# Optimization experiments

Measured on AMD Instinct MI355X. Metric: run time of the kernel, lower is better.

Reference implementation:

```python
import jax, jax.numpy as jnp
import numpy as np

TAU = 2.0      # LIF membrane time constant
VTH = 1.0      # spiking threshold (spikingjelly default)
ALPHA = 4.0    # surrogate sigmoid sharpness (spikingjelly Sigmoid default)
EPS = 1e-5     # BatchNorm eps


@jax.custom_vjp
def spike(v):
    # Heaviside(v) with surrogate sigmoid gradient
    return (v >= 0.0).astype(v.dtype)

def _spike_fwd(v):
    return spike(v), v

def _spike_bwd(v, g):
    s = jax.nn.sigmoid(ALPHA * v)
    return (g * ALPHA * s * (1.0 - s),)

spike.defvjp(_spike_fwd, _spike_bwd)


def lif(x_seq):
    # MultiStepLIFNode: x_seq [T, B, C], v_reset=0 (hard reset), detach_reset=True
    def step(v, xt):
        v = v + (xt - v) / TAU           # membrane decay + charge
        s = spike(v - VTH)               # fire
        v = v * (1.0 - jax.lax.stop_gradient(s))  # detached hard reset to 0
        return v, s
    v0 = jnp.zeros_like(x_seq[0])
    _, s_seq = jax.lax.scan(step, v0, x_seq)
    return s_seq


def block(h, w, b, gamma, beta):
    # h: [B, C_in, T] -> conv1d(k=3, pad=1) -> BN (batch stats) -> LIF -> [B, E, T]
    y = jax.lax.conv_general_dilated(h, w, window_strides=(1,), padding=[(1, 1)],
                                     dimension_numbers=('NCH', 'OIH', 'NCH'))
    y = y + b[None, :, None]
    mu = y.mean(axis=(0, 2), keepdims=True)
    var = y.var(axis=(0, 2), keepdims=True)
    y = (y - mu) * jax.lax.rsqrt(var + EPS) * gamma[None, :, None] + beta[None, :, None]
    s = lif(jnp.transpose(y, (2, 0, 1)))        # [T, B, E]
    return jnp.transpose(s, (1, 2, 0))          # [B, E, T]


def setup_inputs() -> dict:
    key = jax.random.key(0)
    ks = jax.random.split(key, 8)
    B, T, Cin, E, O = 64, 1024, 8, 256, 63
    return {
        'x':       jax.random.normal(ks[0], (B, T, Cin), jnp.float32),
        'conv0_w': jax.random.normal(ks[1], (E, Cin, 3), jnp.float32) * (1.0 / np.sqrt(Cin * 3)),
        'conv0_b': jax.random.normal(ks[2], (E,), jnp.float32) * 0.01,
        'convs_w': jax.random.normal(ks[3], (3, E, E, 3), jnp.float32) * (1.0 / np.sqrt(E * 3)),
        'convs_b': jax.random.normal(ks[4], (3, E), jnp.float32) * 0.01,
        'bn_gamma': jnp.ones((4, E), jnp.float32),
        'bn_beta':  jnp.zeros((4, E), jnp.float32),
        'head_w':  jax.random.normal(ks[5], (O, E), jnp.float32) * (1.0 / np.sqrt(E)),
        'head_b':  jnp.zeros((O,), jnp.float32),
    }


def reference(x, conv0_w, conv0_b, convs_w, convs_b, bn_gamma, bn_beta, head_w, head_b):
    h = jnp.transpose(x, (0, 2, 1))  # [B, C, T]
    h = block(h, conv0_w, conv0_b, bn_gamma[0], bn_beta[0])
    for i in range(convs_w.shape[0]):
        h = block(h, convs_w[i], convs_b[i], bn_gamma[i + 1], bn_beta[i + 1])
    h = h.mean(axis=-1)  # AdaptiveAvgPool1d(1) + squeeze -> [B, E]
    return h @ head_w.T + head_b  # [B, O]
```

## Files before the change

### kernel.cpp

```cpp
#include <hip/hip_runtime.h>
#include <hip/hip_bf16.h>
#include <stdint.h>

#define NB 64
#define NT 1024
#define CIN 8
#define NE 256
#define NO 63
#define TPAD 16
#define TROWS (NT + 2*TPAD)
#define LCH 128
#define LWU 48
#define TT 256

using bf16x8 = __attribute__((ext_vector_type(8))) short;
using f32x4  = __attribute__((ext_vector_type(4))) float;

__global__ void conv0_prep(const float* __restrict__ x, const float* __restrict__ w0,
                           const float* __restrict__ b0, float* __restrict__ y,
                           float* __restrict__ part,
                           const float* __restrict__ cw, __hip_bfloat16* __restrict__ wfr) {
    int bid = blockIdx.x;
    if (bid >= 512) {
        int F = (bid - 512) * 256 + threadIdx.x;
        int lane = F & 63;
        int xx = F >> 6;
        int cph = xx & 7;  xx >>= 3;
        int e4  = xx & 15; xx >>= 4;
        int s   = xx & 1;  xx >>= 1;
        int k   = xx % 3;
        int l   = xx / 3;
        int e = e4*16 + (lane & 15);
        int cb = cph*32 + (lane >> 4)*8;
        __hip_bfloat16 outv[8];
        #pragma unroll
        for (int j = 0; j < 8; ++j) {
            float w = cw[((size_t)(l*256 + e)*256 + (cb + j))*3 + k];
            __hip_bfloat16 hi = __float2bfloat16(w);
            if (s == 0) outv[j] = hi;
            else        outv[j] = __float2bfloat16(w - __bfloat162float(hi));
        }
        *(uint4*)(wfr + (size_t)F*8) = *(uint4*)outv;
        return;
    }
    int b = bid >> 3, tc = bid & 7;
    int e = threadIdx.x;
    int t0 = tc * 128;
    __shared__ float xs[1040];
    for (int i = threadIdx.x; i < 1040; i += 256) {
        int t = t0 - 1 + (i >> 3); int c = i & 7;
        xs[i] = (t >= 0 && t < NT) ? x[((size_t)b*NT + t)*CIN + c] : 0.0f;
    }
    __syncthreads();
    float w[24];
    #pragma unroll
    for (int j = 0; j < 24; ++j) w[j] = w0[e*24 + j];
    float bias = b0[e];
    float s = 0.0f, qq = 0.0f;
    for (int dt = 0; dt < 128; ++dt) {
        float acc = bias;
        #pragma unroll
        for (int c = 0; c < 8; ++c)
            #pragma unroll
            for (int k = 0; k < 3; ++k)
                acc += xs[(dt + k)*8 + c] * w[c*3 + k];
        y[((size_t)b*NT + t0 + dt)*NE + e] = acc;
        s += acc; qq += acc*acc;
    }
    int p = b*8 + tc;
    part[(size_t)p*512 + e]       = s;
    part[(size_t)p*512 + 256 + e] = qq;
}

__global__ void stats_final(const float* __restrict__ part, const float* __restrict__ gamma,
                            const float* __restrict__ beta, float4* __restrict__ lifp, int np) {
    int e = blockIdx.x; int lane = threadIdx.x;
    double s = 0.0, q = 0.0;
    for (int p = lane; p < np; p += 64) {
        s += (double)part[(size_t)p*512 + e];
        q += (double)part[(size_t)p*512 + 256 + e];
    }
    #pragma unroll
    for (int off = 1; off < 64; off <<= 1) {
        s += __shfl_xor(s, off, 64);
        q += __shfl_xor(q, off, 64);
    }
    if (lane == 0) {
        const double N = 65536.0;
        double mean = s / N;
        double var  = q / N - mean*mean;
        float rs = (float)(1.0 / sqrt(var + 1e-5));
        float4 o; o.x = (float)mean; o.y = rs * gamma[e]; o.z = beta[e]; o.w = 0.0f;
        lifp[e] = o;
    }
}

template<bool WS>
__global__ void lif_kern(const float* __restrict__ y, const float4* __restrict__ lifp,
                         __hip_bfloat16* __restrict__ S, float* __restrict__ pool) {
    int c = blockIdx.x, b = blockIdx.y;
    int e = threadIdx.x;
    float4 pr = lifp[e];
    float mu = pr.x, rsg = pr.y, bet = pr.z;
    const __hip_bfloat16 z   = __float2bfloat16(0.0f);
    const __hip_bfloat16 one = __float2bfloat16(1.0f);
    if (WS) {
        if (c == 0) {
            for (int r = 0; r < TPAD; ++r) S[((size_t)b*TROWS + r)*NE + e] = z;
        }
        if (c == 7) {
            for (int r = 0; r < TPAD; ++r) S[((size_t)b*TROWS + TPAD + NT + r)*NE + e] = z;
        }
    }
    int t0 = c * LCH;
    int tw = t0 - LWU; if (tw < 0) tw = 0;
    const float* yb = y + (size_t)b*NT*NE + e;
    __hip_bfloat16* sb = S + ((size_t)b*TROWS + TPAD)*NE + e;
    float v = 0.0f;
    #pragma unroll 8
    for (int t = tw; t < t0; ++t) {
        float xx = yb[(size_t)t*NE];
        float yn = (xx - mu)*rsg + bet;
        float d  = __fsub_rn(yn, v);
        v = __fadd_rn(v, __fmul_rn(d, 0.5f));
        v = (v >= 1.0f) ? 0.0f : v;
    }
    float cnt = 0.0f;
    #pragma unroll 8
    for (int t = t0; t < t0 + LCH; ++t) {
        float xx = yb[(size_t)t*NE];
        float yn = (xx - mu)*rsg + bet;
        float d  = __fsub_rn(yn, v);
        v = __fadd_rn(v, __fmul_rn(d, 0.5f));
        bool sp = (v >= 1.0f);
        if (WS) sb[(size_t)t*NE] = sp ? one : z;
        else    cnt += sp ? 1.0f : 0.0f;
        v = sp ? 0.0f : v;
    }
    if (!WS) pool[(size_t)(b*8 + c)*256 + e] = cnt;
}

__global__ __launch_bounds__(256, 2) void conv_mfma(
    const __hip_bfloat16* __restrict__ Sp,
    const __hip_bfloat16* __restrict__ Wfr,
    const float* __restrict__ bias,
    float* __restrict__ y,
    float* __restrict__ part)
{
    __shared__ short Bbuf[260*32];
    const int tid  = threadIdx.x;
    const int wave = tid >> 6, lane = tid & 63;
    const int n16  = lane & 15, q = lane >> 4;
    const int we = wave & 1, wt = wave >> 1;
    const int tt = blockIdx.x, et = blockIdx.y, b = blockIdx.z;
    const int t0 = tt * TT;

    f32x4 acc[4][8] = {};
    bf16x8 bfr[8];

    const __hip_bfloat16* Sbase = Sp + ((size_t)b*TROWS + (TPAD - 1 + t0)) * NE;

    for (int ph = 0; ph < 8; ++ph) {
        const int c0 = ph * 32;
        __syncthreads();
        for (int idx = tid; idx < 258*4; idx += 256) {
            int r = idx >> 2, sg = idx & 3;
            uint4 d = *(const uint4*)(Sbase + (size_t)r*NE + c0 + sg*8);
            int sgs = sg ^ ((r >> 1) & 3);
            *(uint4*)((char*)Bbuf + r*64 + sgs*16) = d;
        }
        __syncthreads();
        #pragma unroll 1
        for (int kk = 0; kk < 3; ++kk) {
            #pragma unroll
            for (int g = 0; g < 8; ++g) {
                int row = wt*128 + g*16 + n16 + kk;
                int sgs = q ^ ((row >> 1) & 3);
                bfr[g] = *(const bf16x8*)((const char*)Bbuf + row*64 + sgs*16);
            }
            #pragma unroll
            for (int s = 0; s < 2; ++s) {
                const __hip_bfloat16* wb = Wfr
                    + ((((size_t)(kk*2 + s)*16 + (et*8 + we*4))*8 + ph) << 9) + lane*8;
                bf16x8 afr[4];
                #pragma unroll
                for (int f = 0; f < 4; ++f)
                    afr[f] = *(const bf16x8*)(wb + ((size_t)f << 12));
                #pragma unroll
                for (int f = 0; f < 4; ++f)
                    #pragma unroll
                    for (int g = 0; g < 8; ++g)
                        acc[f][g] = __builtin_amdgcn_mfma_f32_16x16x32_bf16(afr[f], bfr[g], acc[f][g], 0, 0, 0);
            }
        }
    }

    float ls[16] = {}, lq[16] = {};
    float4 bv[4];
    #pragma unroll
    for (int f = 0; f < 4; ++f) bv[f] = *(const float4*)(bias + et*128 + we*64 + f*16 + q*4);
    #pragma unroll
    for (int g = 0; g < 8; ++g) {
        int t = t0 + wt*128 + g*16 + n16;
        float* yt = y + ((size_t)b*NT + t)*NE + et*128 + we*64 + q*4;
        #pragma unroll
        for (int f = 0; f < 4; ++f) {
            f32x4 a = acc[f][g];
            float4 o;
            o.x = a[0] + bv[f].x; o.y = a[1] + bv[f].y; o.z = a[2] + bv[f].z; o.w = a[3] + bv[f].w;
            *(float4*)(yt + f*16) = o;
            ls[f*4+0] += o.x; lq[f*4+0] += o.x*o.x;
            ls[f*4+1] += o.y; lq[f*4+1] += o.y*o.y;
            ls[f*4+2] += o.z; lq[f*4+2] += o.z*o.z;
            ls[f*4+3] += o.w; lq[f*4+3] += o.w*o.w;
        }
    }
    #pragma unroll
    for (int off = 1; off < 16; off <<= 1) {
        #pragma unroll
        for (int i = 0; i < 16; ++i) {
            ls[i] += __shfl_xor(ls[i], off, 64);
            lq[i] += __shfl_xor(lq[i], off, 64);
        }
    }
    __syncthreads();
    float* red = (float*)Bbuf;
    if (n16 == 0 && wt == 0) {
        #pragma unroll
        for (int f = 0; f < 4; ++f)
            #pragma unroll
            for (int r = 0; r < 4; ++r) {
                int el = we*64 + f*16 + q*4 + r;
                red[el] = ls[f*4+r]; red[128+el] = lq[f*4+r];
            }
    }
    __syncthreads();
    if (n16 == 0 && wt == 1) {
        #pragma unroll
        for (int f = 0; f < 4; ++f)
            #pragma unroll
            for (int r = 0; r < 4; ++r) {
                int el = we*64 + f*16 + q*4 + r;
                red[el] += ls[f*4+r]; red[128+el] += lq[f*4+r];
            }
    }
    __syncthreads();
    if (tid < 128) {
        int p = b*4 + tt;
        part[(size_t)p*512 + et*128 + tid]       = red[tid];
        part[(size_t)p*512 + 256 + et*128 + tid] = red[128 + tid];
    }
}

__global__ void head_final(const float* __restrict__ pool, const float* __restrict__ hw,
                           const float* __restrict__ hb, float* __restrict__ out) {
    int b = blockIdx.x;
    int tid = threadIdx.x;
    __shared__ float pooled[256];
    float s = 0.0f;
    #pragma unroll
    for (int c = 0; c < 8; ++c) s += pool[(size_t)(b*8 + c)*256 + tid];
    pooled[tid] = s * (1.0f/1024.0f);
    __syncthreads();
    if (tid < NO) {
        float acc = hb[tid];
        for (int c = 0; c < 256; ++c) acc += pooled[c] * hw[tid*256 + c];
        out[b*NO + tid] = acc;
    }
}

extern "C" void kernel_launch(void* const* d_in, const int* in_sizes, int n_in,
                              void* d_out, int out_size, void* d_ws, size_t ws_size,
                              hipStream_t stream) {
    (void)in_sizes; (void)n_in; (void)out_size; (void)ws_size;
    const float* x       = (const float*)d_in[0];
    const float* conv0_w = (const float*)d_in[1];
    const float* conv0_b = (const float*)d_in[2];
    const float* convs_w = (const float*)d_in[3];
    const float* convs_b = (const float*)d_in[4];
    const float* bn_g    = (const float*)d_in[5];
    const float* bn_b    = (const float*)d_in[6];
    const float* head_w  = (const float*)d_in[7];
    const float* head_b  = (const float*)d_in[8];
    float* out = (float*)d_out;

    char* ws = (char*)d_ws;
    float*          y      = (float*)ws;
    __hip_bfloat16* S      = (__hip_bfloat16*)(ws + 67108864);
    __hip_bfloat16* Wfr    = (__hip_bfloat16*)(ws + 101711872);
    float*          part   = (float*)(ws + 104071168);
    float4*         lifp   = (float4*)(ws + 105119744);
    float*          pool   = (float*)(ws + 105123840);

    conv0_prep<<<1088, 256, 0, stream>>>(x, conv0_w, conv0_b, y, part, convs_w, Wfr);
    stats_final<<<256, 64, 0, stream>>>(part, bn_g, bn_b, lifp, 512);
    lif_kern<true><<<dim3(8, 64), 256, 0, stream>>>(y, lifp, S, nullptr);

    for (int l = 0; l < 3; ++l) {
        conv_mfma<<<dim3(4, 2, 64), 256, 0, stream>>>(S, Wfr + (size_t)l*393216,
                                                      convs_b + l*256, y, part);
        stats_final<<<256, 64, 0, stream>>>(part, bn_g + (l+1)*256, bn_b + (l+1)*256, lifp, 256);
        if (l < 2) lif_kern<true ><<<dim3(8, 64), 256, 0, stream>>>(y, lifp, S, nullptr);
        else       lif_kern<false><<<dim3(8, 64), 256, 0, stream>>>(y, lifp, S, pool);
    }
    head_final<<<64, 256, 0, stream>>>(pool, head_w, head_b, out);
}
```

Baseline: 367.6 us.

## Switch conv MFMA to 32x32x16 tiles and transpose BN partial-sum layout

```diff
diff --git a/kernel.cpp b/kernel.cpp
--- a/kernel.cpp
+++ b/kernel.cpp
@@ -15,6 +15,8 @@
 
 using bf16x8 = __attribute__((ext_vector_type(8))) short;
 using f32x4  = __attribute__((ext_vector_type(4))) float;
+using f32x16 = __attribute__((ext_vector_type(16))) float;
+
 
 __global__ void conv0_prep(const float* __restrict__ x, const float* __restrict__ w0,
                            const float* __restrict__ b0, float* __restrict__ y,
@@ -25,13 +27,13 @@
         int F = (bid - 512) * 256 + threadIdx.x;
         int lane = F & 63;
         int xx = F >> 6;
-        int cph = xx & 7;  xx >>= 3;
-        int e4  = xx & 15; xx >>= 4;
-        int s   = xx & 1;  xx >>= 1;
-        int k   = xx % 3;
-        int l   = xx / 3;
-        int e = e4*16 + (lane & 15);
-        int cb = cph*32 + (lane >> 4)*8;
+        int cchunk = xx & 15; xx >>= 4;
+        int e8     = xx & 7;  xx >>= 3;
+        int s      = xx & 1;  xx >>= 1;
+        int k      = xx % 3;
+        int l      = xx / 3;
+        int e = e8*32 + (lane & 31);
+        int cb = cchunk*16 + (lane >> 5)*8;
         __hip_bfloat16 outv[8];
         #pragma unroll
         for (int j = 0; j < 8; ++j) {
@@ -68,8 +70,8 @@
         s += acc; qq += acc*acc;
     }
     int p = b*8 + tc;
-    part[(size_t)p*512 + e]       = s;
-    part[(size_t)p*512 + 256 + e] = qq;
+    part[(size_t)e*512 + p]         = s;
+    part[(size_t)(256 + e)*512 + p] = qq;
 }
 
 __global__ void stats_final(const float* __restrict__ part, const float* __restrict__ gamma,
@@ -77,8 +79,8 @@
     int e = blockIdx.x; int lane = threadIdx.x;
     double s = 0.0, q = 0.0;
     for (int p = lane; p < np; p += 64) {
-        s += (double)part[(size_t)p*512 + e];
-        q += (double)part[(size_t)p*512 + 256 + e];
+        s += (double)part[(size_t)e*512 + p];
+        q += (double)part[(size_t)(256 + e)*512 + p];
     }
     #pragma unroll
     for (int off = 1; off < 64; off <<= 1) {
@@ -150,13 +152,12 @@
     __shared__ short Bbuf[260*32];
     const int tid  = threadIdx.x;
     const int wave = tid >> 6, lane = tid & 63;
-    const int n16  = lane & 15, q = lane >> 4;
+    const int n32  = lane & 31, h = lane >> 5;
     const int we = wave & 1, wt = wave >> 1;
     const int tt = blockIdx.x, et = blockIdx.y, b = blockIdx.z;
     const int t0 = tt * TT;
 
-    f32x4 acc[4][8] = {};
-    bf16x8 bfr[8];
+    f32x16 acc[2][4] = {};
 
     const __hip_bfloat16* Sbase = Sp + ((size_t)b*TROWS + (TPAD - 1 + t0)) * NE;
 
@@ -172,83 +173,109 @@
         __syncthreads();
         #pragma unroll 1
         for (int kk = 0; kk < 3; ++kk) {
-            #pragma unroll
-            for (int g = 0; g < 8; ++g) {
-                int row = wt*128 + g*16 + n16 + kk;
-                int sgs = q ^ ((row >> 1) & 3);
-                bfr[g] = *(const bf16x8*)((const char*)Bbuf + row*64 + sgs*16);
-            }
+            bf16x8 bfr[2][4];
+            #pragma unroll
+            for (int cc2 = 0; cc2 < 2; ++cc2)
+                #pragma unroll
+                for (int g = 0; g < 4; ++g) {
+                    int row = wt*128 + g*32 + n32 + kk;
+                    int sg = cc2*2 + h;
+                    int sgs = sg ^ ((row >> 1) & 3);
+                    bfr[cc2][g] = *(const bf16x8*)((const char*)Bbuf + row*64 + sgs*16);
+                }
             #pragma unroll
             for (int s = 0; s < 2; ++s) {
                 const __hip_bfloat16* wb = Wfr
-                    + ((((size_t)(kk*2 + s)*16 + (et*8 + we*4))*8 + ph) << 9) + lane*8;
-                bf16x8 afr[4];
+                    + ((((size_t)(kk*2 + s)*8 + (et*4 + we*2))*16 + ph*2) << 9) + lane*8;
+                bf16x8 afr[2][2];
                 #pragma unroll
-                for (int f = 0; f < 4; ++f)
-                    afr[f] = *(const bf16x8*)(wb + ((size_t)f << 12));
+                for (int cc2 = 0; cc2 < 2; ++cc2)
+                    #pragma unroll
+                    for (int f = 0; f < 2; ++f)
+                        afr[cc2][f] = *(const bf16x8*)(wb + (((size_t)f*16 + cc2) << 9));
                 #pragma unroll
-                for (int f = 0; f < 4; ++f)
+                for (int cc2 = 0; cc2 < 2; ++cc2)
                     #pragma unroll
-                    for (int g = 0; g < 8; ++g)
-                        acc[f][g] = __builtin_amdgcn_mfma_f32_16x16x32_bf16(afr[f], bfr[g], acc[f][g], 0, 0, 0);
-            }
-        }
-    }
-
-    float ls[16] = {}, lq[16] = {};
-    float4 bv[4];
-    #pragma unroll
-    for (int f = 0; f < 4; ++f) bv[f] = *(const float4*)(bias + et*128 + we*64 + f*16 + q*4);
-    #pragma unroll
-    for (int g = 0; g < 8; ++g) {
-        int t = t0 + wt*128 + g*16 + n16;
-        float* yt = y + ((size_t)b*NT + t)*NE + et*128 + we*64 + q*4;
-        #pragma unroll
-        for (int f = 0; f < 4; ++f) {
-            f32x4 a = acc[f][g];
-            float4 o;
-            o.x = a[0] + bv[f].x; o.y = a[1] + bv[f].y; o.z = a[2] + bv[f].z; o.w = a[3] + bv[f].w;
-            *(float4*)(yt + f*16) = o;
-            ls[f*4+0] += o.x; lq[f*4+0] += o.x*o.x;
-            ls[f*4+1] += o.y; lq[f*4+1] += o.y*o.y;
-            ls[f*4+2] += o.z; lq[f*4+2] += o.z*o.z;
-            ls[f*4+3] += o.w; lq[f*4+3] += o.w*o.w;
-        }
-    }
-    #pragma unroll
-    for (int off = 1; off < 16; off <<= 1) {
-        #pragma unroll
-        for (int i = 0; i < 16; ++i) {
-            ls[i] += __shfl_xor(ls[i], off, 64);
-            lq[i] += __shfl_xor(lq[i], off, 64);
-        }
+                    for (int f = 0; f < 2; ++f)
+                        #pragma unroll
+                        for (int g = 0; g < 4; ++g)
+                            acc[f][g] = __builtin_amdgcn_mfma_f32_32x32x16_bf16(afr[cc2][f], bfr[cc2][g], acc[f][g], 0, 0, 0);
+            }
+        }
+    }
+
+    float ls[2][16], lq[2][16];
+    #pragma unroll
+    for (int f = 0; f < 2; ++f)
+        #pragma unroll
+        for (int i = 0; i < 16; ++i) { ls[f][i] = 0.0f; lq[f][i] = 0.0f; }
+    #pragma unroll
+    for (int f = 0; f < 2; ++f) {
+        int e_base = et*128 + we*64 + f*32 + 4*h;
+        float4 bv[4];
+        #pragma unroll
+        for (int r4 = 0; r4 < 4; ++r4) bv[r4] = *(const float4*)(bias + e_base + 8*r4);
+        #pragma unroll
+        for (int g = 0; g < 4; ++g) {
+            int t = t0 + wt*128 + g*32 + n32;
+            float* yt = y + ((size_t)b*NT + t)*NE + e_base;
+            #pragma unroll
+            for (int r4 = 0; r4 < 4; ++r4) {
+                float4 o;
+                o.x = acc[f][g][r4*4+0] + bv[r4].x;
+                o.y = acc[f][g][r4*4+1] + bv[r4].y;
+                o.z = acc[f][g][r4*4+2] + bv[r4].z;
+                o.w = acc[f][g][r4*4+3] + bv[r4].w;
+                *(float4*)(yt + 8*r4) = o;
+                ls[f][r4*4+0] += o.x; lq[f][r4*4+0] += o.x*o.x;
+                ls[f][r4*4+1] += o.y; lq[f][r4*4+1] += o.y*o.y;
+                ls[f][r4*4+2] += o.z; lq[f][r4*4+2] += o.z*o.z;
+                ls[f][r4*4+3] += o.w; lq[f][r4*4+3] += o.w*o.w;
+            }
+        }
+    }
+    #pragma unroll
+    for (int off = 1; off < 32; off <<= 1) {
+        #pragma unroll
+        for (int f = 0; f < 2; ++f)
+            #pragma unroll
+            for (int i = 0; i < 16; ++i) {
+                ls[f][i] += __shfl_xor(ls[f][i], off, 64);
+                lq[f][i] += __shfl_xor(lq[f][i], off, 64);
+            }
     }
     __syncthreads();
     float* red = (float*)Bbuf;
-    if (n16 == 0 && wt == 0) {
-        #pragma unroll
-        for (int f = 0; f < 4; ++f)
-            #pragma unroll
-            for (int r = 0; r < 4; ++r) {
-                int el = we*64 + f*16 + q*4 + r;
-                red[el] = ls[f*4+r]; red[128+el] = lq[f*4+r];
-            }
-    }
-    __syncthreads();
-    if (n16 == 0 && wt == 1) {
-        #pragma unroll
-        for (int f = 0; f < 4; ++f)
-            #pragma unroll
-            for (int r = 0; r < 4; ++r) {
-                int el = we*64 + f*16 + q*4 + r;
-                red[el] += ls[f*4+r]; red[128+el] += lq[f*4+r];
+    if (n32 == 0 && wt == 0) {
+        #pragma unroll
+        for (int f = 0; f < 2; ++f)
+            #pragma unroll
+            for (int r4 = 0; r4 < 4; ++r4) {
+                int el = we*64 + f*32 + 4*h + 8*r4;
+                *(float4*)(red + el)       = *(float4*)(&ls[f][r4*4]);
+                *(float4*)(red + 128 + el) = *(float4*)(&lq[f][r4*4]);
+            }
+    }
+    __syncthreads();
+    if (n32 == 0 && wt == 1) {
+        #pragma unroll
+        for (int f = 0; f < 2; ++f)
+            #pragma unroll
+            for (int r4 = 0; r4 < 4; ++r4) {
+                int el = we*64 + f*32 + 4*h + 8*r4;
+                #pragma unroll
+                for (int j = 0; j < 4; ++j) {
+                    red[el + j]       += ls[f][r4*4+j];
+                    red[128 + el + j] += lq[f][r4*4+j];
+                }
             }
     }
     __syncthreads();
     if (tid < 128) {
         int p = b*4 + tt;
-        part[(size_t)p*512 + et*128 + tid]       = red[tid];
-        part[(size_t)p*512 + 256 + et*128 + tid] = red[128 + tid];
+        int e = et*128 + tid;
+        part[(size_t)e*512 + p]         = red[tid];
+        part[(size_t)(256 + e)*512 + p] = red[128 + tid];
     }
 }
 
```

Result: slower. 386.3 us (+5.1%).
